# Kernel optimization log

Measured on AMD Instinct MI355X. Metric: run time of the kernel, lower is better.

Reference implementation:

```python
import jax, jax.numpy as jnp
import numpy as np

N, E, IN, H, G, OUT = 50000, 800000, 128, 128, 64, 10
HEADS, C = 4, 32  # per-head dim = H // HEADS so 4-head concat -> H (keeps chain dims consistent)


def setup_inputs() -> dict:
    key = jax.random.key(0)
    ks = jax.random.split(key, 16)
    p = lambda i, shape: jax.random.normal(ks[i], shape, jnp.float32) * 0.05
    return {
        "x": jax.random.normal(ks[0], (N, IN), jnp.float32),
        "edge_index": jax.random.randint(ks[1], (2, E), 0, N),
        "batch": jnp.sort(jax.random.randint(ks[2], (N,), 0, G)),
        "gcn_W": p(3, (IN, H)), "gcn_b": jnp.zeros((H,), jnp.float32),
        "gat_W": p(4, (H, HEADS * C)),
        "att_src": p(5, (HEADS, C)), "att_dst": p(6, (HEADS, C)),
        "gat_b": jnp.zeros((HEADS * C,), jnp.float32),
        "ec_W1": p(7, (2 * H, 128)), "ec_b1": jnp.zeros((128,), jnp.float32),
        "ec_W2": p(8, (128, H)), "ec_b2": jnp.zeros((H,), jnp.float32),
        "gin_W1": p(9, (H, 128)), "gin_b1": jnp.zeros((128,), jnp.float32),
        "gin_W2": p(10, (128, H)), "gin_b2": jnp.zeros((H,), jnp.float32),
        "gate_W1": p(11, (H, 128)), "gate_b1": jnp.zeros((128,), jnp.float32),
        "gate_W2": p(12, (128, 1)), "gate_b2": jnp.zeros((1,), jnp.float32),
        "fc_W": p(13, (H, OUT)), "fc_b": jnp.zeros((OUT,), jnp.float32),
    }


def reference(x, edge_index, batch, gcn_W, gcn_b, gat_W, att_src, att_dst, gat_b,
              ec_W1, ec_b1, ec_W2, ec_b2, gin_W1, gin_b1, gin_W2, gin_b2,
              gate_W1, gate_b1, gate_W2, gate_b2, fc_W, fc_b):
    src, dst = edge_index[0], edge_index[1]
    loop = jnp.arange(N)
    src_l = jnp.concatenate([src, loop])  # self loops for GCN / GAT
    dst_l = jnp.concatenate([dst, loop])

    deg = jax.ops.segment_sum(jnp.ones_like(dst_l, jnp.float32), dst_l, N)
    dinv = jnp.where(deg > 0, jax.lax.rsqrt(deg), 0.0)
    h = x @ gcn_W
    norm = dinv[src_l] * dinv[dst_l]  # [E+N]
    h = jax.ops.segment_sum(h[src_l] * norm[:, None], dst_l, N) + gcn_b
    h = jax.nn.relu(h)

    # ---- GATConv: 4 heads, per-target edge softmax, concat ----
    g = (h @ gat_W).reshape(N, HEADS, C)
    a_src = (g * att_src).sum(-1)  # [N, HEADS]
    a_dst = (g * att_dst).sum(-1)
    e = jax.nn.leaky_relu(a_src[src_l] + a_dst[dst_l], 0.2)  # [E+N, HEADS]
    e_max = jax.ops.segment_max(e, dst_l, N)
    e = jnp.exp(e - e_max[dst_l])
    e_sum = jax.ops.segment_sum(e, dst_l, N)
    alpha = e / (e_sum[dst_l] + 1e-16)
    h = jax.ops.segment_sum(g[src_l] * alpha[..., None], dst_l, N).reshape(N, HEADS * C) + gat_b
    h = jax.nn.elu(h)

    # ---- EdgeConv: nn([x_i, x_j - x_i]) with max aggregation ----
    msg = jnp.concatenate([h[dst], h[src] - h[dst]], axis=-1)  # [E, 2H]
    msg = jax.nn.relu(msg @ ec_W1 + ec_b1) @ ec_W2 + ec_b2
    agg = jax.ops.segment_max(msg, dst, N)
    h = jax.nn.relu(jnp.where(jnp.isfinite(agg), agg, 0.0))  # isolated nodes -> 0 (PyG scatter-max fill)

    # ---- GINConv (eps=0): nn(x + sum_j x_j) ----
    s = h + jax.ops.segment_sum(h[src], dst, N)
    h = jax.nn.relu(jax.nn.relu(s @ gin_W1 + gin_b1) @ gin_W2 + gin_b2)

    # ---- GlobalAttention pooling: per-graph softmax gating ----
    gate = jax.nn.relu(h @ gate_W1 + gate_b1) @ gate_W2 + gate_b2  # [N, 1]
    gmax = jax.ops.segment_max(gate, batch, G)
    ge = jnp.exp(gate - gmax[batch])
    gsum = jax.ops.segment_sum(ge, batch, G)
    w = ge / (gsum[batch] + 1e-16)
    pooled = jax.ops.segment_sum(w * h, batch, G)  # [G, H]

    out = pooled @ fc_W + fc_b
    return jax.nn.log_softmax(out, axis=1)
```

## Files before the change

### kernel.cpp

```cpp
#include <hip/hip_runtime.h>

#define H 128
#define OUTD 10

typedef short bf16x8 __attribute__((ext_vector_type(8)));
typedef float f32x4 __attribute__((ext_vector_type(4)));

__device__ __forceinline__ unsigned short f2bf(float x) {
  unsigned u = __float_as_uint(x);
  u += 0x7fffu + ((u >> 16) & 1u);
  return (unsigned short)(u >> 16);
}
__device__ __forceinline__ unsigned pack2bf(float a, float b) {
  return (unsigned)f2bf(a) | ((unsigned)f2bf(b) << 16);
}
__device__ __forceinline__ float bf2f(unsigned short u) {
  return __uint_as_float(((unsigned)u) << 16);
}
__device__ __forceinline__ float bflo(unsigned u) { return __uint_as_float(u << 16); }
__device__ __forceinline__ float bfhi(unsigned u) { return __uint_as_float(u & 0xffff0000u); }

__device__ __forceinline__ unsigned fenc(float x) {
  unsigned u = __float_as_uint(x);
  return (u & 0x80000000u) ? ~u : (u | 0x80000000u);
}
__device__ __forceinline__ float fdec(unsigned u) {
  u = (u & 0x80000000u) ? (u & 0x7fffffffu) : ~u;
  return __uint_as_float(u);
}

__global__ void prep_w(const float* __restrict__ gcnW, const float* __restrict__ gatW,
                       const float* __restrict__ ecW1, const float* __restrict__ ecW2,
                       const float* __restrict__ ginW1, const float* __restrict__ ginW2,
                       const float* __restrict__ gtW1, unsigned short* __restrict__ WT) {
  int f = blockIdx.x * 256 + threadIdx.x;
  if (f >= 8 * 16384) return;
  int m = f >> 14, idx = f & 16383;
  int j = idx >> 7, k = idx & 127;
  int src = k * 128 + j;
  float v;
  switch (m) {
    case 0: v = gcnW[src]; break;
    case 1: v = gatW[src]; break;
    case 2: v = ecW1[src] - ecW1[16384 + src]; break;
    case 3: v = ecW1[16384 + src]; break;
    case 4: v = ecW2[src]; break;
    case 5: v = ginW1[src]; break;
    case 6: v = ginW2[src]; break;
    default: v = gtW1[src]; break;
  }
  WT[f] = f2bf(v);
}

template <int IN_BF, int RELU, int BIAS>
__global__ __launch_bounds__(256) void dense_mfma(const void* __restrict__ Xv,
                                                  const unsigned short* __restrict__ WT,
                                                  const float* __restrict__ bias,
                                                  unsigned short* __restrict__ Y, int n) {
  __shared__ unsigned short tile[64][136];
  const int tid = threadIdx.x, lane = tid & 63, wave = tid >> 6;
  const int jl = lane & 15, kg = lane >> 4;
  const int base = blockIdx.x * 64;
  if (base >= n) return;
  const int nr = min(64, n - base);
  if (IN_BF) {
    const uint4* X4 = (const uint4*)Xv;
#pragma unroll
    for (int it = 0; it < 4; ++it) {
      int f = it * 256 + tid, r = f >> 4, q = f & 15;
      if (r < nr) *(uint4*)&tile[r][q * 8] = X4[(size_t)(base + r) * 16 + q];
    }
  } else {
    const float* X = (const float*)Xv;
#pragma unroll
    for (int it = 0; it < 16; ++it) {
      int f = it * 256 + tid, r = f >> 6, kp = f & 63;
      if (r < nr) {
        float2 v = *(const float2*)&X[(size_t)(base + r) * H + 2 * kp];
        *(unsigned*)&tile[r][2 * kp] = pack2bf(v.x, v.y);
      }
    }
  }
  __syncthreads();
  bf16x8 afrag[4];
#pragma unroll
  for (int kk = 0; kk < 4; ++kk)
    afrag[kk] = *(const bf16x8*)&tile[wave * 16 + jl][kk * 32 + kg * 8];
  f32x4 acc[8];
#pragma unroll
  for (int jt = 0; jt < 8; ++jt) {
    f32x4 c = {0.f, 0.f, 0.f, 0.f};
#pragma unroll
    for (int kk = 0; kk < 4; ++kk) {
      bf16x8 bf = *(const bf16x8*)&WT[(size_t)(jt * 16 + jl) * H + kk * 32 + kg * 8];
      c = __builtin_amdgcn_mfma_f32_16x16x32_bf16(afrag[kk], bf, c, 0, 0, 0);
    }
    if (BIAS) {
      float bb = bias[jt * 16 + jl];
#pragma unroll
      for (int r = 0; r < 4; ++r) c[r] += bb;
    }
    if (RELU) {
#pragma unroll
      for (int r = 0; r < 4; ++r) c[r] = fmaxf(c[r], 0.f);
    }
    acc[jt] = c;
  }
  __syncthreads();
#pragma unroll
  for (int jt = 0; jt < 8; ++jt)
#pragma unroll
    for (int r = 0; r < 4; ++r) tile[wave * 16 + kg * 4 + r][jt * 16 + jl] = f2bf(acc[jt][r]);
  __syncthreads();
#pragma unroll
  for (int it = 0; it < 4; ++it) {
    int f = it * 256 + tid, r = f >> 4, q = f & 15;
    if (r < nr) *(uint4*)&Y[(size_t)(base + r) * H + q * 8] = *(const uint4*)&tile[r][q * 8];
  }
}

__global__ __launch_bounds__(256) void dense_dual(const unsigned short* __restrict__ X,
                                                  const unsigned short* __restrict__ WT1,
                                                  const unsigned short* __restrict__ WT2,
                                                  const float* __restrict__ bias2,
                                                  unsigned short* __restrict__ Y1,
                                                  unsigned short* __restrict__ Y2, int n) {
  __shared__ unsigned short tile[64][136];
  const int tid = threadIdx.x, lane = tid & 63, wave = tid >> 6;
  const int jl = lane & 15, kg = lane >> 4;
  const int base = blockIdx.x * 64;
  if (base >= n) return;
  const int nr = min(64, n - base);
  const uint4* X4 = (const uint4*)X;
#pragma unroll
  for (int it = 0; it < 4; ++it) {
    int f = it * 256 + tid, r = f >> 4, q = f & 15;
    if (r < nr) *(uint4*)&tile[r][q * 8] = X4[(size_t)(base + r) * 16 + q];
  }
  __syncthreads();
  bf16x8 afrag[4];
#pragma unroll
  for (int kk = 0; kk < 4; ++kk)
    afrag[kk] = *(const bf16x8*)&tile[wave * 16 + jl][kk * 32 + kg * 8];
  f32x4 acc[8];
#pragma unroll
  for (int jt = 0; jt < 8; ++jt) {
    f32x4 c = {0.f, 0.f, 0.f, 0.f};
#pragma unroll
    for (int kk = 0; kk < 4; ++kk) {
      bf16x8 bf = *(const bf16x8*)&WT1[(size_t)(jt * 16 + jl) * H + kk * 32 + kg * 8];
      c = __builtin_amdgcn_mfma_f32_16x16x32_bf16(afrag[kk], bf, c, 0, 0, 0);
    }
    acc[jt] = c;
  }
  __syncthreads();
#pragma unroll
  for (int jt = 0; jt < 8; ++jt)
#pragma unroll
    for (int r = 0; r < 4; ++r) tile[wave * 16 + kg * 4 + r][jt * 16 + jl] = f2bf(acc[jt][r]);
  __syncthreads();
#pragma unroll
  for (int it = 0; it < 4; ++it) {
    int f = it * 256 + tid, r = f >> 4, q = f & 15;
    if (r < nr) *(uint4*)&Y1[(size_t)(base + r) * H + q * 8] = *(const uint4*)&tile[r][q * 8];
  }
  __syncthreads();
#pragma unroll
  for (int jt = 0; jt < 8; ++jt) {
    f32x4 c = {0.f, 0.f, 0.f, 0.f};
#pragma unroll
    for (int kk = 0; kk < 4; ++kk) {
      bf16x8 bf = *(const bf16x8*)&WT2[(size_t)(jt * 16 + jl) * H + kk * 32 + kg * 8];
      c = __builtin_amdgcn_mfma_f32_16x16x32_bf16(afrag[kk], bf, c, 0, 0, 0);
    }
    float bb = bias2[jt * 16 + jl];
#pragma unroll
    for (int r = 0; r < 4; ++r) c[r] += bb;
    acc[jt] = c;
  }
  __syncthreads();
#pragma unroll
  for (int jt = 0; jt < 8; ++jt)
#pragma unroll
    for (int r = 0; r < 4; ++r) tile[wave * 16 + kg * 4 + r][jt * 16 + jl] = f2bf(acc[jt][r]);
  __syncthreads();
#pragma unroll
  for (int it = 0; it < 4; ++it) {
    int f = it * 256 + tid, r = f >> 4, q = f & 15;
    if (r < nr) *(uint4*)&Y2[(size_t)(base + r) * H + q * 8] = *(const uint4*)&tile[r][q * 8];
  }
}

__global__ void zero_int(int* p, int n) {
  int i = blockIdx.x * 256 + threadIdx.x;
  if (i < n) p[i] = 0;
}
__global__ void csr_count(const int* __restrict__ ei, int* __restrict__ cnt, int E) {
  int e = blockIdx.x * 256 + threadIdx.x;
  if (e < E) atomicAdd(&cnt[ei[(size_t)E + e]], 1);
}
__global__ __launch_bounds__(1024) void scan50k(const int* __restrict__ cnt,
                                                int* __restrict__ row_ptr, int n) {
  __shared__ int ls[1024];
  int t = threadIdx.x;
  int chunk = (n + 1023) >> 10;
  int a = t * chunk;
  if (a > n) a = n;
  int b = a + chunk;
  if (b > n) b = n;
  int s = 0;
  for (int i = a; i < b; ++i) s += cnt[i];
  ls[t] = s;
  __syncthreads();
  for (int off = 1; off < 1024; off <<= 1) {
    int v = (t >= off) ? ls[t - off] : 0;
    __syncthreads();
    ls[t] += v;
    __syncthreads();
  }
  int run = (t > 0) ? ls[t - 1] : 0;
  for (int i = a; i < b; ++i) {
    row_ptr[i] = run;
    run += cnt[i];
  }
  if (t == 1023) row_ptr[n] = ls[1023];
}
__global__ void copy_int(const int* __restrict__ a, int* __restrict__ b, int n) {
  int i = blockIdx.x * 256 + threadIdx.x;
  if (i < n) b[i] = a[i];
}
__global__ void csr_fill(const int* __restrict__ ei, int* __restrict__ cursor,
                         int* __restrict__ csr_src, int* __restrict__ csr_dst, int E) {
  int e = blockIdx.x * 256 + threadIdx.x;
  if (e >= E) return;
  int s = ei[e], d = ei[(size_t)E + e];
  int p = atomicAdd(&cursor[d], 1);
  csr_src[p] = s;
  csr_dst[p] = d;
}
__global__ void dinv_kernel(const int* __restrict__ row_ptr, float* __restrict__ dinv, int n) {
  int i = blockIdx.x * 256 + threadIdx.x;
  if (i < n) dinv[i] = rsqrtf((float)(1 + row_ptr[i + 1] - row_ptr[i]));
}
__global__ void fill_u32(unsigned* p, unsigned v, size_t n) {
  size_t i = (size_t)blockIdx.x * 256 + threadIdx.x;
  if (i < n) p[i] = v;
}

__global__ __launch_bounds__(256) void gcn_gather(const unsigned short* __restrict__ h,
                                                  const float* __restrict__ dinv,
                                                  const int* __restrict__ row_ptr,
                                                  const int* __restrict__ csr_src,
                                                  const float* __restrict__ bias,
                                                  unsigned short* __restrict__ out, int n) {
  int node = blockIdx.x * 4 + (threadIdx.x >> 6);
  int lane = threadIdx.x & 63;
  if (node >= n) return;
  const unsigned* hu = (const unsigned*)h;
  float di = dinv[node];
  unsigned v = hu[(size_t)node * 64 + lane];
  float t0 = bflo(v) * di, t1 = bfhi(v) * di;
  int a = row_ptr[node], b = row_ptr[node + 1];
  for (int e = a; e < b; ++e) {
    int s = csr_src[e];
    float ds = dinv[s];
    unsigned w = hu[(size_t)s * 64 + lane];
    t0 = fmaf(bflo(w), ds, t0);
    t1 = fmaf(bfhi(w), ds, t1);
  }
  float y0 = fmaxf(fmaf(t0, di, bias[lane * 2]), 0.f);
  float y1 = fmaxf(fmaf(t1, di, bias[lane * 2 + 1]), 0.f);
  ((unsigned*)out)[(size_t)node * 64 + lane] = pack2bf(y0, y1);
}

__global__ void att_pre(const unsigned short* __restrict__ g, const float* __restrict__ attS,
                        const float* __restrict__ attD, float* __restrict__ asrc,
                        float* __restrict__ adst, int n) {
  int t = blockIdx.x * 256 + threadIdx.x;
  if (t >= n * 4) return;
  int i = t >> 2, hd = t & 3;
  const unsigned* gr = (const unsigned*)(g + (size_t)i * H + hd * 32);
  float s1 = 0.f, s2 = 0.f;
#pragma unroll
  for (int p = 0; p < 16; ++p) {
    unsigned u = gr[p];
    float a = bflo(u), b = bfhi(u);
    s1 = fmaf(a, attS[hd * 32 + 2 * p], fmaf(b, attS[hd * 32 + 2 * p + 1], s1));
    s2 = fmaf(a, attD[hd * 32 + 2 * p], fmaf(b, attD[hd * 32 + 2 * p + 1], s2));
  }
  asrc[t] = s1;
  adst[t] = s2;
}

__global__ __launch_bounds__(128) void gat_gather(const unsigned short* __restrict__ g,
                                                  const float* __restrict__ asrc,
                                                  const float* __restrict__ adst,
                                                  const int* __restrict__ row_ptr,
                                                  const int* __restrict__ csr_src,
                                                  const float* __restrict__ bias,
                                                  unsigned short* __restrict__ out, int n) {
  __shared__ float wl[32][4];
  __shared__ int sl[32];
  int i = blockIdx.x, t = threadIdx.x;
  int a = row_ptr[i], b = row_ptr[i + 1];
  int c = t, chd = c >> 5;
  float adc = adst[i * 4 + chd];
  float e0 = asrc[i * 4 + chd] + adc;
  e0 = e0 > 0.f ? e0 : 0.2f * e0;
  float w = __expf(e0);
  float acc = w * bf2f(g[(size_t)i * H + c]);
  float wsum = w;
  for (int cb = a; cb < b; cb += 32) {
    int m = min(32, b - cb);
    __syncthreads();
    if (t < 4 * m) {
      int el = t >> 2, hd = t & 3;
      int s = csr_src[cb + el];
      float ev = asrc[s * 4 + hd] + adst[i * 4 + hd];
      ev = ev > 0.f ? ev : 0.2f * ev;
      wl[el][hd] = __expf(ev);
      if (hd == 0) sl[el] = s;
    }
    __syncthreads();
    for (int el = 0; el < m; ++el) {
      int s = sl[el];
      float we = wl[el][chd];
      acc = fmaf(we, bf2f(g[(size_t)s * H + c]), acc);
      wsum += we;
    }
  }
  float r = acc / (wsum + 1e-16f) + bias[c];
  out[(size_t)i * H + c] = f2bf(r > 0.f ? r : expm1f(r));
}

__global__ __launch_bounds__(256) void edgeconv_mfma(const unsigned short* __restrict__ A,
                                                     const unsigned short* __restrict__ Bm,
                                                     const int* __restrict__ csr_src,
                                                     const int* __restrict__ csr_dst,
                                                     const unsigned short* __restrict__ W2T,
                                                     const float* __restrict__ b2,
                                                     unsigned* __restrict__ hec, int E) {
  __shared__ unsigned short tile[64][136];
  __shared__ int dsts[64];
  const int tid = threadIdx.x, lane = tid & 63, wave = tid >> 6;
  const int jl = lane & 15, kg = lane >> 4;
  const float b2c = b2[tid & 127];
  for (int base = blockIdx.x * 64; base < E; base += gridDim.x * 64) {
    const int ne = min(64, E - base);
    __syncthreads();
#pragma unroll
    for (int it = 0; it < 8; ++it) {
      int f = it * 256 + tid, r = f >> 5, q = f & 31;
      if (r < ne) {
        int s = csr_src[base + r], d = csr_dst[base + r];
        uint2 va = *(const uint2*)&A[(size_t)d * H + q * 4];
        uint2 vb = *(const uint2*)&Bm[(size_t)s * H + q * 4];
        float x0 = fmaxf(bflo(va.x) + bflo(vb.x), 0.f);
        float x1 = fmaxf(bfhi(va.x) + bfhi(vb.x), 0.f);
        float x2 = fmaxf(bflo(va.y) + bflo(vb.y), 0.f);
        float x3 = fmaxf(bfhi(va.y) + bfhi(vb.y), 0.f);
        uint2 o;
        o.x = pack2bf(x0, x1);
        o.y = pack2bf(x2, x3);
        *(uint2*)&tile[r][q * 4] = o;
      }
    }
    if (tid < 64) dsts[tid] = (tid < ne) ? csr_dst[base + tid] : -1;
    __syncthreads();
    bf16x8 afrag[4];
#pragma unroll
    for (int kk = 0; kk < 4; ++kk)
      afrag[kk] = *(const bf16x8*)&tile[wave * 16 + jl][kk * 32 + kg * 8];
    f32x4 acc[8];
#pragma unroll
    for (int jt = 0; jt < 8; ++jt) {
      f32x4 c = {0.f, 0.f, 0.f, 0.f};
#pragma unroll
      for (int kk = 0; kk < 4; ++kk) {
        bf16x8 bf = *(const bf16x8*)&W2T[(size_t)(jt * 16 + jl) * H + kk * 32 + kg * 8];
        c = __builtin_amdgcn_mfma_f32_16x16x32_bf16(afrag[kk], bf, c, 0, 0, 0);
      }
      acc[jt] = c;
    }
    __syncthreads();
#pragma unroll
    for (int jt = 0; jt < 8; ++jt)
#pragma unroll
      for (int r = 0; r < 4; ++r) tile[wave * 16 + kg * 4 + r][jt * 16 + jl] = f2bf(acc[jt][r]);
    __syncthreads();
    {
      const int col = tid & 127, half = tid >> 7;
      int r0 = half * 32, r1 = min(ne, r0 + 32);
      if (r0 < r1) {
        int cur = dsts[r0];
        float m = bf2f(tile[r0][col]);
        for (int r = r0 + 1; r < r1; ++r) {
          int d = dsts[r];
          float v = bf2f(tile[r][col]);
          if (d != cur) {
            atomicMax(&hec[(size_t)cur * H + col], fenc(m + b2c));
            cur = d;
            m = v;
          } else {
            m = fmaxf(m, v);
          }
        }
        atomicMax(&hec[(size_t)cur * H + col], fenc(m + b2c));
      }
    }
  }
}

__global__ __launch_bounds__(256) void gin_gather(const unsigned* __restrict__ hec,
                                                  const int* __restrict__ row_ptr,
                                                  const int* __restrict__ csr_src,
                                                  unsigned short* __restrict__ out, int n) {
  int node = blockIdx.x * 4 + (threadIdx.x >> 6);
  int lane = threadIdx.x & 63;
  if (node >= n) return;
  uint2 v = *(const uint2*)&hec[(size_t)node * H + lane * 2];
  float t0 = fdec(v.x), t1 = fdec(v.y);
  int a = row_ptr[node], b = row_ptr[node + 1];
  for (int e = a; e < b; ++e) {
    int s = csr_src[e];
    uint2 w = *(const uint2*)&hec[(size_t)s * H + lane * 2];
    t0 += fdec(w.x);
    t1 += fdec(w.y);
  }
  ((unsigned*)out)[(size_t)node * 64 + lane] = pack2bf(t0, t1);
}

__global__ __launch_bounds__(256) void gate_dot(const unsigned short* __restrict__ X,
                                                const float* __restrict__ w2,
                                                const float* __restrict__ b2,
                                                float* __restrict__ gate, int n) {
  int wid = (blockIdx.x * 256 + threadIdx.x) >> 6;
  int lane = threadIdx.x & 63;
  if (wid >= n) return;
  unsigned u = ((const unsigned*)X)[(size_t)wid * 64 + lane];
  float a = fmaf(bflo(u), w2[lane * 2], bfhi(u) * w2[lane * 2 + 1]);
#pragma unroll
  for (int off = 32; off; off >>= 1) a += __shfl_xor(a, off);
  if (lane == 0) gate[wid] = a + b2[0];
}
__global__ void starts_kernel(const int* __restrict__ batch, int* __restrict__ starts, int n,
                              int G) {
  int i = blockIdx.x * 256 + threadIdx.x;
  if (i >= n) return;
  int b = batch[i];
  int bp = (i == 0) ? -1 : batch[i - 1];
  for (int g = bp + 1; g <= b; ++g) starts[g] = i;
  if (i == n - 1)
    for (int g = b + 1; g <= G; ++g) starts[g] = n;
}
__global__ __launch_bounds__(256) void pool_fused(float* __restrict__ gate,
                                                  const unsigned short* __restrict__ h4,
                                                  const int* __restrict__ starts,
                                                  const float* __restrict__ fcW,
                                                  const float* __restrict__ fcB,
                                                  float* __restrict__ out) {
  __shared__ float red[256];
  __shared__ float pl[128];
  int g = blockIdx.x, t = threadIdx.x;
  int s0 = starts[g], s1 = starts[g + 1];
  float m = -1e30f;
  for (int i = s0 + t; i < s1; i += 256) m = fmaxf(m, gate[i]);
  red[t] = m;
  __syncthreads();
  for (int off = 128; off; off >>= 1) {
    if (t < off) red[t] = fmaxf(red[t], red[t + off]);
    __syncthreads();
  }
  m = red[0];
  __syncthreads();
  float sm = 0.f;
  for (int i = s0 + t; i < s1; i += 256) {
    float ge = __expf(gate[i] - m);
    gate[i] = ge;
    sm += ge;
  }
  red[t] = sm;
  __syncthreads();
  for (int off = 128; off; off >>= 1) {
    if (t < off) red[t] += red[t + off];
    __syncthreads();
  }
  float inv = 1.f / (red[0] + 1e-16f);
  __syncthreads();
  int c = t & 127, half = t >> 7;
  float acc = 0.f;
  for (int i = s0 + half; i < s1; i += 2) acc = fmaf(gate[i], bf2f(h4[(size_t)i * H + c]), acc);
  red[t] = acc;
  __syncthreads();
  if (t < 128) pl[t] = (red[t] + red[t + 128]) * inv;
  __syncthreads();
  if (t < OUTD) {
    float o = fcB[t];
    for (int k = 0; k < 128; ++k) o = fmaf(pl[k], fcW[k * OUTD + t], o);
    red[t] = o;
  }
  __syncthreads();
  if (t == 0) {
    float mm = -1e30f;
    for (int j = 0; j < OUTD; ++j) mm = fmaxf(mm, red[j]);
    float s = 0.f;
    for (int j = 0; j < OUTD; ++j) s += __expf(red[j] - mm);
    float l = logf(s);
    for (int j = 0; j < OUTD; ++j) out[g * OUTD + j] = red[j] - mm - l;
  }
}

extern "C" void kernel_launch(void* const* d_in, const int* in_sizes, int n_in, void* d_out,
                              int out_size, void* d_ws, size_t ws_size, hipStream_t stream) {
  const float* x = (const float*)d_in[0];
  const int* ei = (const int*)d_in[1];
  const int* batch = (const int*)d_in[2];
  const float* gcnW = (const float*)d_in[3];
  const float* gcnB = (const float*)d_in[4];
  const float* gatW = (const float*)d_in[5];
  const float* attS = (const float*)d_in[6];
  const float* attD = (const float*)d_in[7];
  const float* gatB = (const float*)d_in[8];
  const float* ecW1 = (const float*)d_in[9];
  const float* ecB1 = (const float*)d_in[10];
  const float* ecW2 = (const float*)d_in[11];
  const float* ecB2 = (const float*)d_in[12];
  const float* ginW1 = (const float*)d_in[13];
  const float* ginB1 = (const float*)d_in[14];
  const float* ginW2 = (const float*)d_in[15];
  const float* ginB2 = (const float*)d_in[16];
  const float* gtW1 = (const float*)d_in[17];
  const float* gtB1 = (const float*)d_in[18];
  const float* gtW2 = (const float*)d_in[19];
  const float* gtB2 = (const float*)d_in[20];
  const float* fcW = (const float*)d_in[21];
  const float* fcB = (const float*)d_in[22];

  const int N = in_sizes[0] / H;
  const int E = in_sizes[1] / 2;
  const int G = out_size / OUTD;
  const size_t NH = (size_t)N * H;

  auto align16 = [](char* p) { return (char*)(((uintptr_t)p + 15) & ~(uintptr_t)15); };
  char* p = (char*)d_ws;
  unsigned* hec = (unsigned*)p;      p += NH * 4;
  float* dinv = (float*)p;           p += (size_t)N * 4;
  float* asrc = (float*)p;           p += (size_t)4 * N * 4;
  float* adst = (float*)p;           p += (size_t)4 * N * 4;
  float* gate = (float*)p;           p += (size_t)N * 4;
  int* starts = (int*)p;             p += (size_t)(G + 1) * 4;
  int* cnt = (int*)p;                p += (size_t)N * 4;
  int* row_ptr = (int*)p;            p += (size_t)(N + 1) * 4;
  int* cursor = (int*)p;             p += (size_t)N * 4;
  int* csr_src = (int*)p;            p += (size_t)E * 4;
  int* csr_dst = (int*)p;            p += (size_t)E * 4;
  p = align16(p);
  unsigned short* WT = (unsigned short*)p;  p += (size_t)8 * 16384 * 2;
  p = align16(p);
  unsigned short* T0 = (unsigned short*)p;  p += NH * 2;
  p = align16(p);
  unsigned short* T1 = (unsigned short*)p;  p += NH * 2;
  p = align16(p);
  unsigned short* T2 = (unsigned short*)p;  p += NH * 2;

  const unsigned short* gcnT = WT;
  const unsigned short* gatT = WT + 16384;
  const unsigned short* WaT = WT + 2 * 16384;
  const unsigned short* WbT = WT + 3 * 16384;
  const unsigned short* W2T = WT + 4 * 16384;
  const unsigned short* gin1T = WT + 5 * 16384;
  const unsigned short* gin2T = WT + 6 * 16384;
  const unsigned short* gt1T = WT + 7 * 16384;

  const int gN = (N + 255) / 256;
  const int gNH = (int)((NH + 255) / 256);
  const int gE = (E + 255) / 256;
  const int gDense = (N + 63) / 64;
  const int gW4 = (N + 3) / 4;

  prep_w<<<(8 * 16384 + 255) / 256, 256, 0, stream>>>(gcnW, gatW, ecW1, ecW2, ginW1, ginW2,
                                                      gtW1, WT);
  zero_int<<<gN, 256, 0, stream>>>(cnt, N);
  csr_count<<<gE, 256, 0, stream>>>(ei, cnt, E);
  scan50k<<<1, 1024, 0, stream>>>(cnt, row_ptr, N);
  copy_int<<<gN, 256, 0, stream>>>(row_ptr, cursor, N);
  csr_fill<<<gE, 256, 0, stream>>>(ei, cursor, csr_src, csr_dst, E);
  dinv_kernel<<<gN, 256, 0, stream>>>(row_ptr, dinv, N);

  dense_mfma<0, 0, 0><<<gDense, 256, 0, stream>>>(x, gcnT, nullptr, T0, N);
  gcn_gather<<<gW4, 256, 0, stream>>>(T0, dinv, row_ptr, csr_src, gcnB, T1, N);

  dense_mfma<1, 0, 0><<<gDense, 256, 0, stream>>>(T1, gatT, nullptr, T2, N);
  att_pre<<<(N * 4 + 255) / 256, 256, 0, stream>>>(T2, attS, attD, asrc, adst, N);
  gat_gather<<<N, 128, 0, stream>>>(T2, asrc, adst, row_ptr, csr_src, gatB, T0, N);

  dense_dual<<<gDense, 256, 0, stream>>>(T0, WaT, WbT, ecB1, T1, T2, N);
  fill_u32<<<gNH, 256, 0, stream>>>(hec, 0x80000000u, NH);
  edgeconv_mfma<<<2048, 256, 0, stream>>>(T1, T2, csr_src, csr_dst, W2T, ecB2, hec, E);

  gin_gather<<<gW4, 256, 0, stream>>>(hec, row_ptr, csr_src, T0, N);
  dense_mfma<1, 1, 1><<<gDense, 256, 0, stream>>>(T0, gin1T, ginB1, T1, N);
  dense_mfma<1, 1, 1><<<gDense, 256, 0, stream>>>(T1, gin2T, ginB2, T2, N);

  dense_mfma<1, 1, 1><<<gDense, 256, 0, stream>>>(T2, gt1T, gtB1, T0, N);
  gate_dot<<<(N * 64 + 255) / 256, 256, 0, stream>>>(T0, gtW2, gtB2, gate, N);
  starts_kernel<<<gN, 256, 0, stream>>>(batch, starts, N, G);
  pool_fused<<<G, 256, 0, stream>>>(gate, T2, starts, fcW, fcB, (float*)d_out);
}
```

Before: 982.0 us.

## Restructure EdgeConv as per-node max without atomics; wave-per-node GAT gather

EdgeConv is rewritten so that each wave owns one destination node. The wave walks that node's CSR neighbours in groups of 16 through MFMA and keeps a running max in registers, which removes the fp32 atomicMax scatter, the fill kernel, the csr_dst array and the float-ordering encode/decode. GAT gather changes from one 128-thread block per node with shared-memory staging and syncs to one wave per node that computes attention weights inline. The GCN and GIN gathers unroll the neighbour loop by four to raise memory-level parallelism. The risk is that nodes with few neighbours waste part of each 16-row MFMA tile, and the EdgeConv result is now stored in bf16 rather than fp32.

New measurement: 976.0 us. About the same (-0.6%).

```diff
diff --git a/kernel.cpp b/kernel.cpp
--- a/kernel.cpp
+++ b/kernel.cpp
@@ -19,15 +19,6 @@
 }
 __device__ __forceinline__ float bflo(unsigned u) { return __uint_as_float(u << 16); }
 __device__ __forceinline__ float bfhi(unsigned u) { return __uint_as_float(u & 0xffff0000u); }
-
-__device__ __forceinline__ unsigned fenc(float x) {
-  unsigned u = __float_as_uint(x);
-  return (u & 0x80000000u) ? ~u : (u | 0x80000000u);
-}
-__device__ __forceinline__ float fdec(unsigned u) {
-  u = (u & 0x80000000u) ? (u & 0x7fffffffu) : ~u;
-  return __uint_as_float(u);
-}
 
 __global__ void prep_w(const float* __restrict__ gcnW, const float* __restrict__ gatW,
                        const float* __restrict__ ecW1, const float* __restrict__ ecW2,
@@ -230,21 +221,16 @@
   if (i < n) b[i] = a[i];
 }
 __global__ void csr_fill(const int* __restrict__ ei, int* __restrict__ cursor,
-                         int* __restrict__ csr_src, int* __restrict__ csr_dst, int E) {
+                         int* __restrict__ csr_src, int E) {
   int e = blockIdx.x * 256 + threadIdx.x;
   if (e >= E) return;
   int s = ei[e], d = ei[(size_t)E + e];
   int p = atomicAdd(&cursor[d], 1);
   csr_src[p] = s;
-  csr_dst[p] = d;
 }
 __global__ void dinv_kernel(const int* __restrict__ row_ptr, float* __restrict__ dinv, int n) {
   int i = blockIdx.x * 256 + threadIdx.x;
   if (i < n) dinv[i] = rsqrtf((float)(1 + row_ptr[i + 1] - row_ptr[i]));
-}
-__global__ void fill_u32(unsigned* p, unsigned v, size_t n) {
-  size_t i = (size_t)blockIdx.x * 256 + threadIdx.x;
-  if (i < n) p[i] = v;
 }
 
 __global__ __launch_bounds__(256) void gcn_gather(const unsigned short* __restrict__ h,
@@ -261,7 +247,22 @@
   unsigned v = hu[(size_t)node * 64 + lane];
   float t0 = bflo(v) * di, t1 = bfhi(v) * di;
   int a = row_ptr[node], b = row_ptr[node + 1];
-  for (int e = a; e < b; ++e) {
+  int e = a;
+  for (; e + 4 <= b; e += 4) {
+    int s0 = csr_src[e], s1 = csr_src[e + 1], s2 = csr_src[e + 2], s3 = csr_src[e + 3];
+    unsigned w0 = hu[(size_t)s0 * 64 + lane], w1 = hu[(size_t)s1 * 64 + lane];
+    unsigned w2 = hu[(size_t)s2 * 64 + lane], w3 = hu[(size_t)s3 * 64 + lane];
+    float d0 = dinv[s0], d1 = dinv[s1], d2 = dinv[s2], d3 = dinv[s3];
+    t0 = fmaf(bflo(w0), d0, t0);
+    t1 = fmaf(bfhi(w0), d0, t1);
+    t0 = fmaf(bflo(w1), d1, t0);
+    t1 = fmaf(bfhi(w1), d1, t1);
+    t0 = fmaf(bflo(w2), d2, t0);
+    t1 = fmaf(bfhi(w2), d2, t1);
+    t0 = fmaf(bflo(w3), d3, t0);
+    t1 = fmaf(bfhi(w3), d3, t1);
+  }
+  for (; e < b; ++e) {
     int s = csr_src[e];
     float ds = dinv[s];
     unsigned w = hu[(size_t)s * 64 + lane];
@@ -292,140 +293,162 @@
   adst[t] = s2;
 }
 
-__global__ __launch_bounds__(128) void gat_gather(const unsigned short* __restrict__ g,
+__device__ __forceinline__ float lrelu_exp(float v) {
+  v = v > 0.f ? v : 0.2f * v;
+  return __expf(v);
+}
+
+__global__ __launch_bounds__(256) void gat_gather(const unsigned short* __restrict__ g,
                                                   const float* __restrict__ asrc,
                                                   const float* __restrict__ adst,
                                                   const int* __restrict__ row_ptr,
                                                   const int* __restrict__ csr_src,
                                                   const float* __restrict__ bias,
                                                   unsigned short* __restrict__ out, int n) {
-  __shared__ float wl[32][4];
-  __shared__ int sl[32];
-  int i = blockIdx.x, t = threadIdx.x;
-  int a = row_ptr[i], b = row_ptr[i + 1];
-  int c = t, chd = c >> 5;
-  float adc = adst[i * 4 + chd];
-  float e0 = asrc[i * 4 + chd] + adc;
-  e0 = e0 > 0.f ? e0 : 0.2f * e0;
-  float w = __expf(e0);
-  float acc = w * bf2f(g[(size_t)i * H + c]);
-  float wsum = w;
-  for (int cb = a; cb < b; cb += 32) {
-    int m = min(32, b - cb);
-    __syncthreads();
-    if (t < 4 * m) {
-      int el = t >> 2, hd = t & 3;
-      int s = csr_src[cb + el];
-      float ev = asrc[s * 4 + hd] + adst[i * 4 + hd];
-      ev = ev > 0.f ? ev : 0.2f * ev;
-      wl[el][hd] = __expf(ev);
-      if (hd == 0) sl[el] = s;
-    }
-    __syncthreads();
-    for (int el = 0; el < m; ++el) {
-      int s = sl[el];
-      float we = wl[el][chd];
-      acc = fmaf(we, bf2f(g[(size_t)s * H + c]), acc);
-      wsum += we;
-    }
-  }
-  float r = acc / (wsum + 1e-16f) + bias[c];
-  out[(size_t)i * H + c] = f2bf(r > 0.f ? r : expm1f(r));
-}
-
-__global__ __launch_bounds__(256) void edgeconv_mfma(const unsigned short* __restrict__ A,
+  int node = blockIdx.x * 4 + (threadIdx.x >> 6);
+  int lane = threadIdx.x & 63;
+  if (node >= n) return;
+  const int hd = lane >> 4;
+  const unsigned* gu = (const unsigned*)g;
+  float adc = adst[node * 4 + hd];
+  float w = lrelu_exp(asrc[node * 4 + hd] + adc);
+  unsigned u = gu[(size_t)node * 64 + lane];
+  float acc0 = w * bflo(u), acc1 = w * bfhi(u), wsum = w;
+  int a = row_ptr[node], b = row_ptr[node + 1];
+  int e = a;
+  for (; e + 4 <= b; e += 4) {
+    int s0 = csr_src[e], s1 = csr_src[e + 1], s2 = csr_src[e + 2], s3 = csr_src[e + 3];
+    unsigned u0 = gu[(size_t)s0 * 64 + lane], u1 = gu[(size_t)s1 * 64 + lane];
+    unsigned u2 = gu[(size_t)s2 * 64 + lane], u3 = gu[(size_t)s3 * 64 + lane];
+    float w0 = lrelu_exp(asrc[s0 * 4 + hd] + adc), w1 = lrelu_exp(asrc[s1 * 4 + hd] + adc);
+    float w2 = lrelu_exp(asrc[s2 * 4 + hd] + adc), w3 = lrelu_exp(asrc[s3 * 4 + hd] + adc);
+    acc0 = fmaf(w0, bflo(u0), acc0);
+    acc1 = fmaf(w0, bfhi(u0), acc1);
+    acc0 = fmaf(w1, bflo(u1), acc0);
+    acc1 = fmaf(w1, bfhi(u1), acc1);
+    acc0 = fmaf(w2, bflo(u2), acc0);
+    acc1 = fmaf(w2, bfhi(u2), acc1);
+    acc0 = fmaf(w3, bflo(u3), acc0);
+    acc1 = fmaf(w3, bfhi(u3), acc1);
+    wsum += w0 + w1 + w2 + w3;
+  }
+  for (; e < b; ++e) {
+    int s = csr_src[e];
+    unsigned us = gu[(size_t)s * 64 + lane];
+    float we = lrelu_exp(asrc[s * 4 + hd] + adc);
+    acc0 = fmaf(we, bflo(us), acc0);
+    acc1 = fmaf(we, bfhi(us), acc1);
+    wsum += we;
+  }
+  float inv = 1.f / (wsum + 1e-16f);
+  float r0 = acc0 * inv + bias[2 * lane];
+  float r1 = acc1 * inv + bias[2 * lane + 1];
+  r0 = r0 > 0.f ? r0 : expm1f(r0);
+  r1 = r1 > 0.f ? r1 : expm1f(r1);
+  ((unsigned*)out)[(size_t)node * 64 + lane] = pack2bf(r0, r1);
+}
+
+__global__ __launch_bounds__(256) void edgeconv_node(const unsigned short* __restrict__ A,
                                                      const unsigned short* __restrict__ Bm,
+                                                     const int* __restrict__ row_ptr,
                                                      const int* __restrict__ csr_src,
-                                                     const int* __restrict__ csr_dst,
                                                      const unsigned short* __restrict__ W2T,
                                                      const float* __restrict__ b2,
-                                                     unsigned* __restrict__ hec, int E) {
-  __shared__ unsigned short tile[64][136];
-  __shared__ int dsts[64];
-  const int tid = threadIdx.x, lane = tid & 63, wave = tid >> 6;
+                                                     unsigned short* __restrict__ out, int n) {
+  int node = blockIdx.x * 4 + (threadIdx.x >> 6);
+  if (node >= n) return;
+  const int lane = threadIdx.x & 63;
   const int jl = lane & 15, kg = lane >> 4;
-  const float b2c = b2[tid & 127];
-  for (int base = blockIdx.x * 64; base < E; base += gridDim.x * 64) {
-    const int ne = min(64, E - base);
-    __syncthreads();
-#pragma unroll
-    for (int it = 0; it < 8; ++it) {
-      int f = it * 256 + tid, r = f >> 5, q = f & 31;
-      if (r < ne) {
-        int s = csr_src[base + r], d = csr_dst[base + r];
-        uint2 va = *(const uint2*)&A[(size_t)d * H + q * 4];
-        uint2 vb = *(const uint2*)&Bm[(size_t)s * H + q * 4];
-        float x0 = fmaxf(bflo(va.x) + bflo(vb.x), 0.f);
-        float x1 = fmaxf(bfhi(va.x) + bfhi(vb.x), 0.f);
-        float x2 = fmaxf(bflo(va.y) + bflo(vb.y), 0.f);
-        float x3 = fmaxf(bfhi(va.y) + bfhi(vb.y), 0.f);
-        uint2 o;
-        o.x = pack2bf(x0, x1);
-        o.y = pack2bf(x2, x3);
-        *(uint2*)&tile[r][q * 4] = o;
+  int a = row_ptr[node], b = row_ptr[node + 1];
+  unsigned* orow = (unsigned*)(out + (size_t)node * H);
+  if (a == b) {
+    if (kg == 0 && !(jl & 1)) {
+#pragma unroll
+      for (int jt = 0; jt < 8; ++jt) orow[jt * 8 + (jl >> 1)] = 0u;
+    }
+    return;
+  }
+  bf16x8 ad[4];
+  const unsigned short* Arow = A + (size_t)node * H;
+#pragma unroll
+  for (int kk = 0; kk < 4; ++kk) ad[kk] = *(const bf16x8*)&Arow[kk * 32 + kg * 8];
+  f32x4 best[8];
+#pragma unroll
+  for (int jt = 0; jt < 8; ++jt) best[jt] = {-1e30f, -1e30f, -1e30f, -1e30f};
+  for (int base = a; base < b; base += 16) {
+    const int m = min(16, b - base);
+    bf16x8 af[4];
+    if (jl < m) {
+      int s = csr_src[base + jl];
+      const unsigned short* Brow = Bm + (size_t)s * H;
+#pragma unroll
+      for (int kk = 0; kk < 4; ++kk) {
+        bf16x8 bv = *(const bf16x8*)&Brow[kk * 32 + kg * 8];
+        bf16x8 o;
+#pragma unroll
+        for (int q = 0; q < 8; ++q) {
+          float xv = bf2f((unsigned short)ad[kk][q]) + bf2f((unsigned short)bv[q]);
+          o[q] = (short)f2bf(fmaxf(xv, 0.f));
+        }
+        af[kk] = o;
       }
-    }
-    if (tid < 64) dsts[tid] = (tid < ne) ? csr_dst[base + tid] : -1;
-    __syncthreads();
-    bf16x8 afrag[4];
-#pragma unroll
-    for (int kk = 0; kk < 4; ++kk)
-      afrag[kk] = *(const bf16x8*)&tile[wave * 16 + jl][kk * 32 + kg * 8];
-    f32x4 acc[8];
+    } else {
+#pragma unroll
+      for (int kk = 0; kk < 4; ++kk) {
+#pragma unroll
+        for (int q = 0; q < 8; ++q) af[kk][q] = 0;
+      }
+    }
 #pragma unroll
     for (int jt = 0; jt < 8; ++jt) {
       f32x4 c = {0.f, 0.f, 0.f, 0.f};
 #pragma unroll
       for (int kk = 0; kk < 4; ++kk) {
-        bf16x8 bf = *(const bf16x8*)&W2T[(size_t)(jt * 16 + jl) * H + kk * 32 + kg * 8];
-        c = __builtin_amdgcn_mfma_f32_16x16x32_bf16(afrag[kk], bf, c, 0, 0, 0);
+        bf16x8 wf = *(const bf16x8*)&W2T[(size_t)(jt * 16 + jl) * H + kk * 32 + kg * 8];
+        c = __builtin_amdgcn_mfma_f32_16x16x32_bf16(af[kk], wf, c, 0, 0, 0);
       }
-      acc[jt] = c;
-    }
-    __syncthreads();
-#pragma unroll
-    for (int jt = 0; jt < 8; ++jt)
-#pragma unroll
-      for (int r = 0; r < 4; ++r) tile[wave * 16 + kg * 4 + r][jt * 16 + jl] = f2bf(acc[jt][r]);
-    __syncthreads();
-    {
-      const int col = tid & 127, half = tid >> 7;
-      int r0 = half * 32, r1 = min(ne, r0 + 32);
-      if (r0 < r1) {
-        int cur = dsts[r0];
-        float m = bf2f(tile[r0][col]);
-        for (int r = r0 + 1; r < r1; ++r) {
-          int d = dsts[r];
-          float v = bf2f(tile[r][col]);
-          if (d != cur) {
-            atomicMax(&hec[(size_t)cur * H + col], fenc(m + b2c));
-            cur = d;
-            m = v;
-          } else {
-            m = fmaxf(m, v);
-          }
-        }
-        atomicMax(&hec[(size_t)cur * H + col], fenc(m + b2c));
+#pragma unroll
+      for (int r = 0; r < 4; ++r) {
+        int row = kg * 4 + r;
+        best[jt][r] = fmaxf(best[jt][r], (row < m) ? c[r] : -1e30f);
       }
     }
   }
-}
-
-__global__ __launch_bounds__(256) void gin_gather(const unsigned* __restrict__ hec,
+#pragma unroll
+  for (int jt = 0; jt < 8; ++jt) {
+    float mv = fmaxf(fmaxf(best[jt][0], best[jt][1]), fmaxf(best[jt][2], best[jt][3]));
+    mv = fmaxf(mv, __shfl_xor(mv, 16));
+    mv = fmaxf(mv, __shfl_xor(mv, 32));
+    float val = fmaxf(mv + b2[jt * 16 + jl], 0.f);
+    float other = __shfl_xor(val, 1);
+    if (kg == 0 && !(jl & 1)) orow[jt * 8 + (jl >> 1)] = pack2bf(val, other);
+  }
+}
+
+__global__ __launch_bounds__(256) void gin_gather(const unsigned short* __restrict__ h,
                                                   const int* __restrict__ row_ptr,
                                                   const int* __restrict__ csr_src,
                                                   unsigned short* __restrict__ out, int n) {
   int node = blockIdx.x * 4 + (threadIdx.x >> 6);
   int lane = threadIdx.x & 63;
   if (node >= n) return;
-  uint2 v = *(const uint2*)&hec[(size_t)node * H + lane * 2];
-  float t0 = fdec(v.x), t1 = fdec(v.y);
+  const unsigned* hu = (const unsigned*)h;
+  unsigned v = hu[(size_t)node * 64 + lane];
+  float t0 = bflo(v), t1 = bfhi(v);
   int a = row_ptr[node], b = row_ptr[node + 1];
-  for (int e = a; e < b; ++e) {
+  int e = a;
+  for (; e + 4 <= b; e += 4) {
+    int s0 = csr_src[e], s1 = csr_src[e + 1], s2 = csr_src[e + 2], s3 = csr_src[e + 3];
+    unsigned w0 = hu[(size_t)s0 * 64 + lane], w1 = hu[(size_t)s1 * 64 + lane];
+    unsigned w2 = hu[(size_t)s2 * 64 + lane], w3 = hu[(size_t)s3 * 64 + lane];
+    t0 += bflo(w0) + bflo(w1) + bflo(w2) + bflo(w3);
+    t1 += bfhi(w0) + bfhi(w1) + bfhi(w2) + bfhi(w3);
+  }
+  for (; e < b; ++e) {
     int s = csr_src[e];
-    uint2 w = *(const uint2*)&hec[(size_t)s * H + lane * 2];
-    t0 += fdec(w.x);
-    t1 += fdec(w.y);
+    unsigned w = hu[(size_t)s * 64 + lane];
+    t0 += bflo(w);
+    t1 += bfhi(w);
   }
   ((unsigned*)out)[(size_t)node * 64 + lane] = pack2bf(t0, t1);
 }
@@ -543,7 +566,6 @@
 
   auto align16 = [](char* p) { return (char*)(((uintptr_t)p + 15) & ~(uintptr_t)15); };
   char* p = (char*)d_ws;
-  unsigned* hec = (unsigned*)p;      p += NH * 4;
   float* dinv = (float*)p;           p += (size_t)N * 4;
   float* asrc = (float*)p;           p += (size_t)4 * N * 4;
   float* adst = (float*)p;           p += (size_t)4 * N * 4;
@@ -553,7 +575,6 @@
   int* row_ptr = (int*)p;            p += (size_t)(N + 1) * 4;
   int* cursor = (int*)p;             p += (size_t)N * 4;
   int* csr_src = (int*)p;            p += (size_t)E * 4;
-  int* csr_dst = (int*)p;            p += (size_t)E * 4;
   p = align16(p);
   unsigned short* WT = (unsigned short*)p;  p += (size_t)8 * 16384 * 2;
   p = align16(p);
@@ -562,6 +583,8 @@
   unsigned short* T1 = (unsigned short*)p;  p += NH * 2;
   p = align16(p);
   unsigned short* T2 = (unsigned short*)p;  p += NH * 2;
+  p = align16(p);
+  unsigned short* T3 = (unsigned short*)p;  p += NH * 2;
 
   const unsigned short* gcnT = WT;
   const unsigned short* gatT = WT + 16384;
@@ -573,7 +596,6 @@
   const unsigned short* gt1T = WT + 7 * 16384;
 
   const int gN = (N + 255) / 256;
-  const int gNH = (int)((NH + 255) / 256);
   const int gE = (E + 255) / 256;
   const int gDense = (N + 63) / 64;
   const int gW4 = (N + 3) / 4;
@@ -584,7 +606,7 @@
   csr_count<<<gE, 256, 0, stream>>>(ei, cnt, E);
   scan50k<<<1, 1024, 0, stream>>>(cnt, row_ptr, N);
   copy_int<<<gN, 256, 0, stream>>>(row_ptr, cursor, N);
-  csr_fill<<<gE, 256, 0, stream>>>(ei, cursor, csr_src, csr_dst, E);
+  csr_fill<<<gE, 256, 0, stream>>>(ei, cursor, csr_src, E);
   dinv_kernel<<<gN, 256, 0, stream>>>(row_ptr, dinv, N);
 
   dense_mfma<0, 0, 0><<<gDense, 256, 0, stream>>>(x, gcnT, nullptr, T0, N);
@@ -592,13 +614,12 @@
 
   dense_mfma<1, 0, 0><<<gDense, 256, 0, stream>>>(T1, gatT, nullptr, T2, N);
   att_pre<<<(N * 4 + 255) / 256, 256, 0, stream>>>(T2, attS, attD, asrc, adst, N);
-  gat_gather<<<N, 128, 0, stream>>>(T2, asrc, adst, row_ptr, csr_src, gatB, T0, N);
+  gat_gather<<<gW4, 256, 0, stream>>>(T2, asrc, adst, row_ptr, csr_src, gatB, T0, N);
 
   dense_dual<<<gDense, 256, 0, stream>>>(T0, WaT, WbT, ecB1, T1, T2, N);
-  fill_u32<<<gNH, 256, 0, stream>>>(hec, 0x80000000u, NH);
-  edgeconv_mfma<<<2048, 256, 0, stream>>>(T1, T2, csr_src, csr_dst, W2T, ecB2, hec, E);
-
-  gin_gather<<<gW4, 256, 0, stream>>>(hec, row_ptr, csr_src, T0, N);
+  edgeconv_node<<<gW4, 256, 0, stream>>>(T1, T2, row_ptr, csr_src, W2T, ecB2, T3, N);
+
+  gin_gather<<<gW4, 256, 0, stream>>>(T3, row_ptr, csr_src, T0, N);
   dense_mfma<1, 1, 1><<<gDense, 256, 0, stream>>>(T0, gin1T, ginB1, T1, N);
   dense_mfma<1, 1, 1><<<gDense, 256, 0, stream>>>(T1, gin2T, ginB2, T2, N);
 
```
